# Kernel optimization log

Hardware: AMD Instinct MI355X
Metric: run time of the kernel (lower is better)

Reference implementation:

```python
import jax, jax.numpy as jnp
import numpy as np

DIM = 512
HEADS = 16
WS = 7  # window size (cube), N = WS**3 = 343
B_ = 128
N = WS ** 3
TABLE = (2 * WS - 1) ** 3  # 2197


def _relative_position_index():
    coords = np.stack(np.meshgrid(np.arange(WS), np.arange(WS), np.arange(WS), indexing='ij'))  # [3,WS,WS,WS]
    cf = coords.reshape(3, -1)  # [3, N]
    rel = cf[:, :, None] - cf[:, None, :]  # [3, N, N]
    rel = rel.transpose(1, 2, 0).copy()
    rel[:, :, 0] += WS - 1
    rel[:, :, 1] += WS - 1
    rel[:, :, 2] += WS - 1
    rel[:, :, 0] *= (2 * WS - 1) * (2 * WS - 1)
    rel[:, :, 1] *= 2 * WS - 1
    return jnp.asarray(rel.sum(-1), dtype=jnp.int32)  # [N, N]


def setup_inputs() -> dict:
    key = jax.random.key(0)
    ks = jax.random.split(key, 8)
    x = jax.random.normal(ks[0], (B_, N, DIM), dtype=jnp.float32)
    q_global = jax.random.normal(ks[1], (1, DIM), dtype=jnp.float32)
    qkv_w = jax.random.normal(ks[2], (3 * DIM, DIM), dtype=jnp.float32) * (DIM ** -0.5)
    qkv_b = jax.random.normal(ks[3], (3 * DIM,), dtype=jnp.float32) * 0.02
    proj_w = jax.random.normal(ks[4], (DIM, DIM), dtype=jnp.float32) * (DIM ** -0.5)
    proj_b = jax.random.normal(ks[5], (DIM,), dtype=jnp.float32) * 0.02
    rel_bias_table = jax.random.normal(ks[6], (TABLE, HEADS), dtype=jnp.float32) * 0.02
    rel_pos_index = _relative_position_index()
    return {"x": x, "q_global": q_global, "qkv_w": qkv_w, "qkv_b": qkv_b,
            "rel_bias_table": rel_bias_table, "proj_w": proj_w, "proj_b": proj_b,
            "rel_pos_index": rel_pos_index}


def reference(x, q_global, qkv_w, qkv_b, rel_bias_table, proj_w, proj_b, rel_pos_index):
    B, Nt, C = x.shape
    hd = C // HEADS
    scale = hd ** -0.5
    # QKV projection (torch Linear: x @ W.T + b)
    qkv = (x @ qkv_w.T + qkv_b).reshape(B, Nt, 3, HEADS, hd)
    qkv = jnp.transpose(qkv, (2, 0, 3, 1, 4))  # [3, B, H, N, hd]
    q, k, v = qkv[0] * scale, qkv[1], qkv[2]
    attn = jnp.einsum('bhqd,bhkd->bhqk', q, k)  # [B, H, N, N]
    # relative position bias gather: table[idx] -> [N, N, H] -> [H, N, N]
    bias = rel_bias_table[rel_pos_index.reshape(-1)].reshape(Nt, Nt, HEADS)
    attn = attn + jnp.transpose(bias, (2, 0, 1))[None]
    attn = jax.nn.softmax(attn, axis=-1)
    out = jnp.einsum('bhqk,bhkd->bhqd', attn, v)  # [B, H, N, hd]
    out = jnp.transpose(out, (0, 2, 1, 3)).reshape(B, Nt, C)
    return out @ proj_w.T + proj_b
```

## Files before the change

kernel.cpp:

```cpp
#include <hip/hip_runtime.h>

typedef unsigned short u16;
typedef __attribute__((ext_vector_type(8))) short short8;
typedef __attribute__((ext_vector_type(4))) float f32x4;
typedef __attribute__((ext_vector_type(4))) unsigned uint4v;

#define NTOK 343
#define DIMC 512
#define HEADS_ 16
#define BATCH 128
#define TBL 117649

#define LOG2E 1.4426950408889634f
#define QSCALE (0.17677669529663687f * LOG2E)

__device__ __forceinline__ u16 f2bf(float f) {
  unsigned u = __builtin_bit_cast(unsigned, f);
  unsigned r = (u + 0x7fffu + ((u >> 16) & 1u)) >> 16;
  return (u16)r;
}
__device__ __forceinline__ float bf2f(u16 x) {
  return __builtin_bit_cast(float, ((unsigned)x) << 16);
}
__device__ __forceinline__ unsigned cvtpk(float lo, float hi) {
  unsigned r;
  asm("v_cvt_pk_bf16_f32 %0, %1, %2" : "=v"(r) : "v"(lo), "v"(hi));
  return r;
}

__global__ void cvt_f32_bf16_k(const float* __restrict__ in, u16* __restrict__ out, int n4) {
  int i = blockIdx.x * blockDim.x + threadIdx.x;
  int st = gridDim.x * blockDim.x;
  for (; i < n4; i += st) {
    float4 v = reinterpret_cast<const float4*>(in)[i];
    ushort4 o;
    o.x = f2bf(v.x); o.y = f2bf(v.y); o.z = f2bf(v.z); o.w = f2bf(v.w);
    reinterpret_cast<ushort4*>(out)[i] = o;
  }
}

__global__ void bias_pre_k(const float* __restrict__ table, const int* __restrict__ idx,
                           u16* __restrict__ biasB) {
  int t = blockIdx.x * 256 + threadIdx.x;
  if (t >= HEADS_ * 22 * 22 * 64) return;
  int l = t & 63;
  int tq = (t >> 6) % 22;
  int nt = ((t >> 6) / 22) % 22;
  int h = (t >> 6) / 484;
  int q = tq * 16 + (l & 15);
  int k0 = nt * 16 + (l >> 4) * 4;
  ushort4 o;
  u16* oe = (u16*)&o;
#pragma unroll
  for (int r = 0; r < 4; ++r) {
    int k = k0 + r;
    float v = (q < NTOK && k < NTOK) ? (LOG2E * table[idx[q * NTOK + k] * HEADS_ + h]) : -1e30f;
    oe[r] = f2bf(v);
  }
  *reinterpret_cast<ushort4*>(biasB + (size_t)t * 4) = o;
}

#define GLD16(gptr, lptr)                                                        \
  __builtin_amdgcn_global_load_lds(                                              \
      (const __attribute__((address_space(1))) void*)(const void*)(gptr),        \
      (__attribute__((address_space(3))) void*)(void*)(lptr), 16, 0, 0)

template <int EPI>
__global__ __launch_bounds__(256) void gemm_bt_k(const u16* __restrict__ A,
                                                 const u16* __restrict__ B,
                                                 const float* __restrict__ bias,
                                                 void* __restrict__ C, int N, int K) {
  const int NBL = N >> 7;
  int nwg = gridDim.x;
  int orig = blockIdx.x;
  int qq = nwg >> 3, rr = nwg & 7;
  int xcd = orig & 7, lid = orig >> 3;
  int bid = (xcd < rr ? xcd * (qq + 1) : rr * (qq + 1) + (xcd - rr) * qq) + lid;
  int mb = bid / NBL, nb = bid % NBL;
  __shared__ __align__(16) u16 As[128 * 64];
  __shared__ __align__(16) u16 Bs[128 * 64];
  int tid = threadIdx.x;
  int w = tid >> 6, l = tid & 63;
  int wr = w >> 1, wc = w & 1;
  f32x4 acc[4][4];
#pragma unroll
  for (int i = 0; i < 4; i++)
#pragma unroll
    for (int j = 0; j < 4; j++) acc[i][j] = (f32x4){0.f, 0.f, 0.f, 0.f};

  const int l8r = l >> 3, l8c = l & 7;
  const u16* Abase = A + (size_t)(mb * 128 + w * 32 + l8r) * K + l8c * 8;
  const u16* Bbase = B + (size_t)(nb * 128 + w * 32 + l8r) * K + l8c * 8;
  u16* AsW = As + (w * 32) * 64;
  u16* BsW = Bs + (w * 32) * 64;

  int KT = K >> 6;
  for (int kt = 0; kt < KT; ++kt) {
#pragma unroll
    for (int i4 = 0; i4 < 4; ++i4) {
      GLD16(Abase + kt * 64 + (size_t)(i4 * 8) * K, AsW + i4 * 512 + l * 8);
      GLD16(Bbase + kt * 64 + (size_t)(i4 * 8) * K, BsW + i4 * 512 + l * 8);
    }
    __syncthreads();
#pragma unroll
    for (int kk = 0; kk < 2; ++kk) {
      short8 af[4], bf[4];
#pragma unroll
      for (int i = 0; i < 4; i++)
        af[i] = *reinterpret_cast<const short8*>(As + (wr * 64 + i * 16 + (l & 15)) * 64 +
                                                 kk * 32 + (l >> 4) * 8);
#pragma unroll
      for (int j = 0; j < 4; j++)
        bf[j] = *reinterpret_cast<const short8*>(Bs + (wc * 64 + j * 16 + (l & 15)) * 64 +
                                                 kk * 32 + (l >> 4) * 8);
#pragma unroll
      for (int i = 0; i < 4; i++)
#pragma unroll
        for (int j = 0; j < 4; j++)
          acc[i][j] = __builtin_amdgcn_mfma_f32_16x16x32_bf16(af[i], bf[j], acc[i][j], 0, 0, 0);
    }
    __syncthreads();
  }
  int r0 = mb * 128 + wr * 64 + (l >> 4) * 4;
  int c0 = nb * 128 + wc * 64 + (l & 15);
#pragma unroll
  for (int j = 0; j < 4; j++) {
    int col = c0 + j * 16;
    float bv = bias[col];
    float mul = (EPI == 0 && col < 512) ? QSCALE : 1.0f;
#pragma unroll
    for (int i = 0; i < 4; i++) {
      int row = r0 + i * 16;
      if (EPI == 0) {
        u16* Cp = (u16*)C + (size_t)row * N + col;
#pragma unroll
        for (int r = 0; r < 4; r += 2) {
          unsigned pk = cvtpk((acc[i][j][r] + bv) * mul, (acc[i][j][r + 1] + bv) * mul);
          Cp[(size_t)r * N] = (u16)pk;
          Cp[(size_t)(r + 1) * N] = (u16)(pk >> 16);
        }
      } else {
#pragma unroll
        for (int r = 0; r < 4; r++)
          ((float*)C)[(size_t)(row + r) * N + col] = acc[i][j][r] + bv;
      }
    }
  }
}

__global__ __launch_bounds__(256, 3) void attn_k(const u16* __restrict__ qkv,
                                                 const u16* __restrict__ biasB,
                                                 u16* __restrict__ outA) {
  int p = blockIdx.x;
  int jj = p >> 3;
  int h = 2 * (p & 7) + (jj >> 7);
  int b = jj & 127;
  __shared__ __align__(16) u16 kS[352 * 40];
  __shared__ __align__(16) u16 vT[32 * 370];
  int tid = threadIdx.x;

  for (int idx = tid; idx < 352 * 4; idx += 256) {
    int row = idx >> 2, seg = idx & 3;
    uint4 vk = {0, 0, 0, 0};
    if (row < NTOK)
      vk = *reinterpret_cast<const uint4*>(qkv + (size_t)(b * NTOK + row) * 1536 + 512 +
                                           h * 32 + seg * 8);
    *reinterpret_cast<uint4*>(kS + row * 40 + seg * 8) = vk;
  }
  for (int idx = tid; idx < NTOK * 4; idx += 256) {
    int row = idx >> 2, seg = idx & 3;
    size_t base = (size_t)(b * NTOK + row) * 1536 + 1024 + h * 32 + seg * 8;
    uint4 vv = *reinterpret_cast<const uint4*>(qkv + base);
    const u16* e = reinterpret_cast<const u16*>(&vv);
#pragma unroll
    for (int t = 0; t < 8; ++t) vT[(seg * 8 + t) * 370 + row] = e[t];
  }
  for (int idx = tid; idx < 32 * 9; idx += 256) vT[(idx / 9) * 370 + NTOK + (idx % 9)] = 0;
  __syncthreads();

  int w = tid >> 6, l = tid & 63;
  const int cl = l & 15, q4 = l >> 4;
  const f32x4 z4 = (f32x4){0.f, 0.f, 0.f, 0.f};
  for (int tq = w; tq < 22; tq += 4) {
    short8 bq = (short8){0, 0, 0, 0, 0, 0, 0, 0};
    int qrow = tq * 16 + cl;
    if (qrow < NTOK)
      bq = *reinterpret_cast<const short8*>(qkv + (size_t)(b * NTOK + qrow) * 1536 + h * 32 +
                                            q4 * 8);
    unsigned pk[22][2];
    float tot = 0.f;
    const u16* bbase = biasB + ((size_t)(h * 22) * 22 + tq) * 256 + l * 4;
#pragma unroll
    for (int nt = 0; nt < 22; ++nt) {
      short8 ak = *reinterpret_cast<const short8*>(kS + (nt * 16 + cl) * 40 + q4 * 8);
      f32x4 s = __builtin_amdgcn_mfma_f32_16x16x32_bf16(ak, bq, z4, 0, 0, 0);
      ushort4 bb = *reinterpret_cast<const ushort4*>(bbase + (size_t)nt * 22 * 256);
      const u16* be = (const u16*)&bb;
      float e0 = __builtin_amdgcn_exp2f(s[0] + bf2f(be[0]));
      float e1 = __builtin_amdgcn_exp2f(s[1] + bf2f(be[1]));
      float e2 = __builtin_amdgcn_exp2f(s[2] + bf2f(be[2]));
      float e3 = __builtin_amdgcn_exp2f(s[3] + bf2f(be[3]));
      tot += (e0 + e1) + (e2 + e3);
      pk[nt][0] = cvtpk(e0, e1);
      pk[nt][1] = cvtpk(e2, e3);
    }
    tot += __builtin_bit_cast(float, __shfl_xor(__builtin_bit_cast(int, tot), 16));
    tot += __builtin_bit_cast(float, __shfl_xor(__builtin_bit_cast(int, tot), 32));
    float inv = 1.0f / tot;
    float ir[4];
#pragma unroll
    for (int r = 0; r < 4; ++r)
      ir[r] = __shfl(inv, q4 * 4 + r);

    f32x4 O0 = z4, O1 = z4;
#pragma unroll
    for (int kt = 0; kt < 11; ++kt) {
      unsigned v16_0 = (q4 & 2) ? pk[2 * kt + 1][0] : pk[2 * kt][0];
      unsigned v16_1 = (q4 & 2) ? pk[2 * kt + 1][1] : pk[2 * kt][1];
      unsigned v32_0 = (q4 & 2) ? pk[2 * kt][0] : pk[2 * kt + 1][0];
      unsigned v32_1 = (q4 & 2) ? pk[2 * kt][1] : pk[2 * kt + 1][1];
      unsigned t1_0 = (unsigned)__shfl_xor((int)v16_0, 16);
      unsigned t1_1 = (unsigned)__shfl_xor((int)v16_1, 16);
      unsigned t2_0 = (unsigned)__shfl_xor((int)v32_0, 32);
      unsigned t2_1 = (unsigned)__shfl_xor((int)v32_1, 32);
      unsigned t3_0 = (unsigned)__shfl_xor((int)t2_0, 16);
      unsigned t3_1 = (unsigned)__shfl_xor((int)t2_1, 16);
      unsigned f0 = (q4 & 1) ? ((q4 & 2) ? t1_0 : t3_0) : ((q4 & 2) ? t2_0 : v16_0);
      unsigned f1 = (q4 & 1) ? ((q4 & 2) ? t1_1 : t3_1) : ((q4 & 2) ? t2_1 : v16_1);
      unsigned s0 = (q4 & 1) ? ((q4 & 2) ? v16_0 : t2_0) : ((q4 & 2) ? t3_0 : t1_0);
      unsigned s1 = (q4 & 1) ? ((q4 & 2) ? v16_1 : t2_1) : ((q4 & 2) ? t3_1 : t1_1);
      uint4v ap = (uint4v){f0, f1, s0, s1};
      short8 bv0 = *reinterpret_cast<const short8*>(vT + cl * 370 + kt * 32 + q4 * 8);
      short8 bv1 = *reinterpret_cast<const short8*>(vT + (16 + cl) * 370 + kt * 32 + q4 * 8);
      O0 = __builtin_amdgcn_mfma_f32_16x16x32_bf16(__builtin_bit_cast(short8, ap), bv0, O0,
                                                   0, 0, 0);
      O1 = __builtin_amdgcn_mfma_f32_16x16x32_bf16(__builtin_bit_cast(short8, ap), bv1, O1,
                                                   0, 0, 0);
    }
#pragma unroll
    for (int r = 0; r < 4; ++r) {
      int qr2 = tq * 16 + q4 * 4 + r;
      if (qr2 < NTOK) {
        unsigned pko = cvtpk(O0[r] * ir[r], O1[r] * ir[r]);
        u16* op = outA + (size_t)(b * NTOK + qr2) * 512 + h * 32 + cl;
        op[0] = (u16)pko;
        op[16] = (u16)(pko >> 16);
      }
    }
  }
}

extern "C" void kernel_launch(void* const* d_in, const int* in_sizes, int n_in,
                              void* d_out, int out_size, void* d_ws, size_t ws_size,
                              hipStream_t stream) {
  const float* x      = (const float*)d_in[0];
  const float* qkv_w  = (const float*)d_in[2];
  const float* qkv_b  = (const float*)d_in[3];
  const float* table  = (const float*)d_in[4];
  const float* proj_w = (const float*)d_in[5];
  const float* proj_b = (const float*)d_in[6];
  const int*   relidx = (const int*)d_in[7];

  char* ws = (char*)d_ws;
  u16*   x_bf  = (u16*)(ws);
  u16*   qw_bf = (u16*)(ws + 44957696);
  u16*   pw_bf = (u16*)(ws + 46530560);
  u16*   qkv_o = (u16*)(ws + 47054848);
  u16*   biasB = (u16*)(ws + 181927936);

  cvt_f32_bf16_k<<<2048, 256, 0, stream>>>(x, x_bf, (BATCH * NTOK * DIMC) / 4);
  cvt_f32_bf16_k<<<768, 256, 0, stream>>>(qkv_w, qw_bf, (3 * DIMC * DIMC) / 4);
  cvt_f32_bf16_k<<<256, 256, 0, stream>>>(proj_w, pw_bf, (DIMC * DIMC) / 4);
  bias_pre_k<<<(HEADS_ * 22 * 22 * 64 + 255) / 256, 256, 0, stream>>>(table, relidx, biasB);

  gemm_bt_k<0><<<343 * 12, 256, 0, stream>>>(x_bf, qw_bf, qkv_b, qkv_o, 1536, 512);
  attn_k<<<BATCH * HEADS_, 256, 0, stream>>>(qkv_o, biasB, x_bf);
  gemm_bt_k<1><<<343 * 4, 256, 0, stream>>>(x_bf, pw_bf, proj_b, d_out, 512, 512);
}
```

Baseline: 311.8 us.

## Replace 128x128 GEMM with 256x256 double-buffered swizzled LDS GEMM

Both projection GEMMs now use a 512-thread kernel with 256x256 output tiles. It double-buffers A and B tiles in a single 128KB LDS array with an XOR swizzle to avoid bank conflicts, prefetches the next K-slab while MFMAs run, and raises wave priority during the compute phase. Row clamping and masked stores handle M=43904, which is not a multiple of 256. The larger tile improves data reuse per load, at the cost of fewer workgroups (1032 and 344), which may leave the tail underutilized on the 512-wide projection.

```diff
diff --git a/kernel.cpp b/kernel.cpp
--- a/kernel.cpp
+++ b/kernel.cpp
@@ -9,6 +9,7 @@
 #define DIMC 512
 #define HEADS_ 16
 #define BATCH 128
+#define MROWS 43904
 #define TBL 117649
 
 #define LOG2E 1.4426950408889634f
@@ -66,83 +67,120 @@
       (__attribute__((address_space(3))) void*)(void*)(lptr), 16, 0, 0)
 
 template <int EPI>
-__global__ __launch_bounds__(256) void gemm_bt_k(const u16* __restrict__ A,
-                                                 const u16* __restrict__ B,
-                                                 const float* __restrict__ bias,
-                                                 void* __restrict__ C, int N, int K) {
-  const int NBL = N >> 7;
+__global__ __launch_bounds__(512, 2) void gemm256_k(const u16* __restrict__ A,
+                                                    const u16* __restrict__ B,
+                                                    const float* __restrict__ bias,
+                                                    void* __restrict__ C, int N, int K, int M) {
+  const int NBL = N >> 8;
   int nwg = gridDim.x;
   int orig = blockIdx.x;
   int qq = nwg >> 3, rr = nwg & 7;
   int xcd = orig & 7, lid = orig >> 3;
   int bid = (xcd < rr ? xcd * (qq + 1) : rr * (qq + 1) + (xcd - rr) * qq) + lid;
   int mb = bid / NBL, nb = bid % NBL;
-  __shared__ __align__(16) u16 As[128 * 64];
-  __shared__ __align__(16) u16 Bs[128 * 64];
+
+  __shared__ __align__(16) u16 lds_[65536];
+
   int tid = threadIdx.x;
   int w = tid >> 6, l = tid & 63;
-  int wr = w >> 1, wc = w & 1;
-  f32x4 acc[4][4];
-#pragma unroll
-  for (int i = 0; i < 4; i++)
-#pragma unroll
-    for (int j = 0; j < 4; j++) acc[i][j] = (f32x4){0.f, 0.f, 0.f, 0.f};
-
-  const int l8r = l >> 3, l8c = l & 7;
-  const u16* Abase = A + (size_t)(mb * 128 + w * 32 + l8r) * K + l8c * 8;
-  const u16* Bbase = B + (size_t)(nb * 128 + w * 32 + l8r) * K + l8c * 8;
-  u16* AsW = As + (w * 32) * 64;
-  u16* BsW = Bs + (w * 32) * 64;
-
-  int KT = K >> 6;
-  for (int kt = 0; kt < KT; ++kt) {
-#pragma unroll
-    for (int i4 = 0; i4 < 4; ++i4) {
-      GLD16(Abase + kt * 64 + (size_t)(i4 * 8) * K, AsW + i4 * 512 + l * 8);
-      GLD16(Bbase + kt * 64 + (size_t)(i4 * 8) * K, BsW + i4 * 512 + l * 8);
-    }
-    __syncthreads();
-#pragma unroll
-    for (int kk = 0; kk < 2; ++kk) {
-      short8 af[4], bf[4];
-#pragma unroll
-      for (int i = 0; i < 4; i++)
-        af[i] = *reinterpret_cast<const short8*>(As + (wr * 64 + i * 16 + (l & 15)) * 64 +
-                                                 kk * 32 + (l >> 4) * 8);
-#pragma unroll
-      for (int j = 0; j < 4; j++)
-        bf[j] = *reinterpret_cast<const short8*>(Bs + (wc * 64 + j * 16 + (l & 15)) * 64 +
-                                                 kk * 32 + (l >> 4) * 8);
-#pragma unroll
-      for (int i = 0; i < 4; i++)
-#pragma unroll
-        for (int j = 0; j < 4; j++)
-          acc[i][j] = __builtin_amdgcn_mfma_f32_16x16x32_bf16(af[i], bf[j], acc[i][j], 0, 0, 0);
-    }
-    __syncthreads();
-  }
-  int r0 = mb * 128 + wr * 64 + (l >> 4) * 4;
-  int c0 = nb * 128 + wc * 64 + (l & 15);
-#pragma unroll
-  for (int j = 0; j < 4; j++) {
+  int wm = w >> 2, wn = w & 3;
+  int cl = l & 15, q4 = l >> 4;
+
+  f32x4 acc[8][4];
+#pragma unroll
+  for (int i = 0; i < 8; ++i)
+#pragma unroll
+    for (int j = 0; j < 4; ++j) acc[i][j] = (f32x4){0.f, 0.f, 0.f, 0.f};
+
+  const int srow = tid >> 3;
+  const int scolb = (tid & 7) * 16;
+
+  const int NT = K >> 6;
+
+#define STG(g, mat, half)                                                                   \
+  {                                                                                         \
+    _Pragma("unroll") for (int rd = 0; rd < 2; ++rd) {                                      \
+      int row = rd * 64 + srow;                                                             \
+      int colb = scolb ^ (((row >> 1) & 7) << 4);            \
+      const u16* src;                                                                       \
+      if (mat == 0) {                                                                       \
+        int gr = mb * 256 + (half)*128 + row;                                               \
+        gr = gr < M ? gr : M - 1;                                                           \
+        src = A + (size_t)gr * K + (g)*64 + (colb >> 1);                                    \
+      } else {                                                                              \
+        int gr = nb * 256 + (half)*128 + row;                                               \
+        src = B + (size_t)gr * K + (g)*64 + (colb >> 1);                                    \
+      }                                                                                     \
+      GLD16(src, lds_ + ((g)&1) * 32768 + (mat)*16384 + (half)*8192 + tid * 8 + rd * 4096); \
+    }                                                                                       \
+  }
+
+  STG(0, 0, 0); STG(0, 0, 1); STG(0, 1, 0); STG(0, 1, 1);
+  asm volatile("s_waitcnt vmcnt(0)" ::: "memory");
+  __builtin_amdgcn_s_barrier();
+
+  for (int g = 0; g < NT; ++g) {
+    const u16* sA = lds_ + (g & 1) * 32768 + wm * 8192;
+    const u16* sB = lds_ + (g & 1) * 32768 + 16384 + (wn >> 1) * 8192;
+#pragma unroll
+    for (int p = 0; p < 4; ++p) {
+      const int mh = p & 1, ks = p >> 1;
+      short8 af[4], bf4[4];
+#pragma unroll
+      for (int m = 0; m < 4; ++m) {
+        int xb = (mh * 64 + m * 16 + cl) * 128 + ks * 64 + q4 * 16;
+        xb ^= ((xb >> 8) & 7) << 4;
+        af[m] = *reinterpret_cast<const short8*>(sA + (xb >> 1));
+      }
+#pragma unroll
+      for (int n = 0; n < 4; ++n) {
+        int xb = ((wn & 1) * 64 + n * 16 + cl) * 128 + ks * 64 + q4 * 16;
+        xb ^= ((xb >> 8) & 7) << 4;
+        bf4[n] = *reinterpret_cast<const short8*>(sB + (xb >> 1));
+      }
+      if (g + 1 < NT) {
+        if (p == 0) { STG(g + 1, 0, 0); STG(g + 1, 0, 1); }
+        else if (p == 1) { STG(g + 1, 1, 0); STG(g + 1, 1, 1); }
+      }
+      __builtin_amdgcn_s_barrier();
+      asm volatile("s_waitcnt lgkmcnt(0)" ::: "memory");
+      __builtin_amdgcn_sched_barrier(0);
+      __builtin_amdgcn_s_setprio(1);
+#pragma unroll
+      for (int m = 0; m < 4; ++m)
+#pragma unroll
+        for (int n = 0; n < 4; ++n)
+          acc[mh * 4 + m][n] =
+              __builtin_amdgcn_mfma_f32_16x16x32_bf16(af[m], bf4[n], acc[mh * 4 + m][n], 0, 0, 0);
+      __builtin_amdgcn_s_setprio(0);
+      if (p == 3) asm volatile("s_waitcnt vmcnt(0)" ::: "memory");
+      __builtin_amdgcn_s_barrier();
+    }
+  }
+#undef STG
+
+  int r0 = mb * 256 + wm * 128 + q4 * 4;
+  int c0 = nb * 256 + wn * 64 + cl;
+#pragma unroll
+  for (int j = 0; j < 4; ++j) {
     int col = c0 + j * 16;
     float bv = bias[col];
     float mul = (EPI == 0 && col < 512) ? QSCALE : 1.0f;
 #pragma unroll
-    for (int i = 0; i < 4; i++) {
+    for (int i = 0; i < 8; ++i) {
       int row = r0 + i * 16;
       if (EPI == 0) {
         u16* Cp = (u16*)C + (size_t)row * N + col;
 #pragma unroll
         for (int r = 0; r < 4; r += 2) {
           unsigned pk = cvtpk((acc[i][j][r] + bv) * mul, (acc[i][j][r + 1] + bv) * mul);
-          Cp[(size_t)r * N] = (u16)pk;
-          Cp[(size_t)(r + 1) * N] = (u16)(pk >> 16);
+          if (row + r < M) Cp[(size_t)r * N] = (u16)pk;
+          if (row + r + 1 < M) Cp[(size_t)(r + 1) * N] = (u16)(pk >> 16);
         }
       } else {
 #pragma unroll
         for (int r = 0; r < 4; r++)
-          ((float*)C)[(size_t)(row + r) * N + col] = acc[i][j][r] + bv;
+          if (row + r < M) ((float*)C)[(size_t)(row + r) * N + col] = acc[i][j][r] + bv;
       }
     }
   }
@@ -273,7 +311,7 @@
   cvt_f32_bf16_k<<<256, 256, 0, stream>>>(proj_w, pw_bf, (DIMC * DIMC) / 4);
   bias_pre_k<<<(HEADS_ * 22 * 22 * 64 + 255) / 256, 256, 0, stream>>>(table, relidx, biasB);
 
-  gemm_bt_k<0><<<343 * 12, 256, 0, stream>>>(x_bf, qw_bf, qkv_b, qkv_o, 1536, 512);
+  gemm256_k<0><<<172 * 6, 512, 0, stream>>>(x_bf, qw_bf, qkv_b, qkv_o, 1536, 512, MROWS);
   attn_k<<<BATCH * HEADS_, 256, 0, stream>>>(qkv_o, biasB, x_bf);
-  gemm_bt_k<1><<<343 * 4, 256, 0, stream>>>(x_bf, pw_bf, proj_b, d_out, 512, 512);
-}
+  gemm256_k<1><<<172 * 2, 512, 0, stream>>>(x_bf, pw_bf, proj_b, d_out, 512, 512, MROWS);
+}
```

After: 339.5 us. +8.9%, slower.
